# Kernel tuning notes

Measured on AMD Instinct MI355X. Metric: run time of the kernel, lower is better.

The kernel has to match this reference:

```python
import jax, jax.numpy as jnp
import numpy as np

DIM = 128
HEADS = 4
DH = 32
SCALE = DH ** -0.5


def _ln(x, g, b):
    m = x.mean(-1, keepdims=True)
    v = x.var(-1, keepdims=True)
    return (x - m) / jnp.sqrt(v + 1e-5) * g + b


def setup_inputs() -> dict:
    key = jax.random.key(0)
    ks = jax.random.split(key, 16)
    B, N, H, W, HK, WK = 2, 6, 48, 48, 24, 24
    d, hd = DIM, HEADS * DH
    p = lambda k, s: (jax.random.normal(k, s, jnp.float32) * 0.02)
    return {
        "q": jax.random.normal(ks[0], (B, N, d, H, W), jnp.float32),
        "k": jax.random.normal(ks[1], (B, N, d, HK, WK), jnp.float32),
        "v": jax.random.normal(ks[2], (B, N, d, HK, WK), jnp.float32),
        "skip": jax.random.normal(ks[3], (B, d, H, W), jnp.float32),
        "lnq_g": jnp.ones(d), "lnq_b": jnp.zeros(d),
        "Wq": p(ks[4], (d, hd)), "bq": jnp.zeros(hd),
        "lnk_g": jnp.ones(d), "lnk_b": jnp.zeros(d),
        "Wk": p(ks[5], (d, hd)), "bk": jnp.zeros(hd),
        "lnv_g": jnp.ones(d), "lnv_b": jnp.zeros(d),
        "Wv": p(ks[6], (d, hd)), "bv": jnp.zeros(hd),
        "Wp": p(ks[7], (hd, d)), "bp": jnp.zeros(d),
        "pre_g": jnp.ones(d), "pre_b": jnp.zeros(d),
        "W1": p(ks[8], (d, 2 * d)), "b1": jnp.zeros(2 * d),
        "W2": p(ks[9], (2 * d, d)), "b2": jnp.zeros(d),
        "post_g": jnp.ones(d), "post_b": jnp.zeros(d),
    }


def reference(q, k, v, skip, lnq_g, lnq_b, Wq, bq, lnk_g, lnk_b, Wk, bk,
              lnv_g, lnv_b, Wv, bv, Wp, bp, pre_g, pre_b, W1, b1, W2, b2,
              post_g, post_b):
    B, N, d, H, W = q.shape
    _, _, _, HK, WK = k.shape
    Q, K = H * W, HK * WK
    # b n d H W -> b n (H W) d
    qx = q.transpose(0, 1, 3, 4, 2).reshape(B, N, Q, d)
    kx = k.transpose(0, 1, 3, 4, 2).reshape(B, N, K, d)
    vx = v.transpose(0, 1, 3, 4, 2).reshape(B, N * K, d)
    # norm + linear projections
    qp = _ln(qx, lnq_g, lnq_b) @ Wq + bq  # (B,N,Q,HEADS*DH)
    kp = _ln(kx, lnk_g, lnk_b) @ Wk + bk
    vp = _ln(vx, lnv_g, lnv_b) @ Wv + bv  # (B,N*K,HEADS*DH)
    # split heads: b ... (m d) -> (b m) ... d
    qp = qp.reshape(B, N, Q, HEADS, DH).transpose(0, 3, 1, 2, 4).reshape(B * HEADS, N, Q, DH)
    kp = kp.reshape(B, N, K, HEADS, DH).transpose(0, 3, 1, 2, 4).reshape(B * HEADS, N, K, DH)
    vp = vp.reshape(B, N * K, HEADS, DH).transpose(0, 2, 1, 3).reshape(B * HEADS, N * K, DH)
    # per-view scores, then softmax jointly over (n K)
    scores = SCALE * jnp.einsum('bnqd,bnkd->bnqk', qp, kp)
    scores = scores.transpose(0, 2, 1, 3).reshape(B * HEADS, Q, N * K)
    a = jax.nn.softmax(scores, axis=-1)
    out = jnp.einsum('bqk,bkd->bqd', a, vp)  # (B*HEADS, Q, DH)
    # merge heads: (b m) Q d -> b Q (m d)
    z = out.reshape(B, HEADS, Q, DH).transpose(0, 2, 1, 3).reshape(B, Q, HEADS * DH)
    z = z @ Wp + bp
    z = z + skip.transpose(0, 2, 3, 1).reshape(B, Q, d)
    z = _ln(z, pre_g, pre_b)
    z = z + (jax.nn.gelu(z @ W1 + b1, approximate=False) @ W2 + b2)
    z = _ln(z, post_g, post_b)
    return z.reshape(B, H, W, d).transpose(0, 3, 1, 2)
```

## Files before the change

kernel.cpp:

```cpp
#include <hip/hip_runtime.h>
#include <cmath>

#define B_    2
#define N_    6
#define D_    128
#define Q_    2304
#define K_    576
#define NK_   3456
#define HEADS_ 4
#define DH_   32
#define SCALE_ 0.17677669529663687f
#define SCLOG2E_ 0.25504672615621814f

typedef __attribute__((ext_vector_type(8))) short bf16x8;
typedef __attribute__((ext_vector_type(4))) float f32x4;

#if defined(__has_builtin)
#if __has_builtin(__builtin_amdgcn_cvt_pk_bf16_f32)
#define HAS_PK_BF16 1
#endif
#endif

static __device__ __forceinline__ unsigned short f2bf(float f) {
  union { float f; unsigned u; } x; x.f = f;
  unsigned u = x.u + 0x7fffu + ((x.u >> 16) & 1u);
  return (unsigned short)(u >> 16);
}
static __device__ __forceinline__ unsigned pkbf(float a, float b) {
#ifdef HAS_PK_BF16
  typedef __attribute__((ext_vector_type(2))) __bf16 vbf2;
  union { vbf2 v; unsigned u; } cv;
  cv.v = __builtin_amdgcn_cvt_pk_bf16_f32(a, b);
  return cv.u;
#else
  return (unsigned)f2bf(a) | ((unsigned)f2bf(b) << 16);
#endif
}

__global__ __launch_bounds__(256) void k_prep_wt(
    const float* __restrict__ Wq, const float* __restrict__ Wk,
    const float* __restrict__ Wv, const float* __restrict__ Wp,
    const float* __restrict__ W1, const float* __restrict__ W2,
    unsigned short* __restrict__ WTq, unsigned short* __restrict__ WTk,
    unsigned short* __restrict__ WTv, unsigned short* __restrict__ WTp,
    unsigned short* __restrict__ WT1, unsigned short* __restrict__ WT2)
{
  __shared__ float tile[32][33];
  const int wb = blockIdx.x, t = threadIdx.x;
  const float* src; unsigned short* dst; int Kd, J, tl;
  if      (wb < 16) { src = Wq; dst = WTq; Kd = 128; J = 128; tl = wb; }
  else if (wb < 32) { src = Wk; dst = WTk; Kd = 128; J = 128; tl = wb - 16; }
  else if (wb < 48) { src = Wv; dst = WTv; Kd = 128; J = 128; tl = wb - 32; }
  else if (wb < 64) { src = Wp; dst = WTp; Kd = 128; J = 128; tl = wb - 48; }
  else if (wb < 96) { src = W1; dst = WT1; Kd = 128; J = 256; tl = wb - 64; }
  else              { src = W2; dst = WT2; Kd = 256; J = 128; tl = wb - 96; }
  const int njt = J >> 5;
  const int tj = tl % njt, tk = tl / njt;
#pragma unroll
  for (int i = 0; i < 4; ++i) {
    int idx = t + 256 * i;
    int r = idx >> 5, c = idx & 31;
    tile[r][c] = src[(size_t)(tk * 32 + r) * J + tj * 32 + c];
  }
  __syncthreads();
#pragma unroll
  for (int i = 0; i < 2; ++i) {
    int idx = t + 256 * i;
    int rr = idx >> 4, c2 = (idx & 15) << 1;
    *(unsigned*)&dst[(size_t)(tj * 32 + rr) * Kd + tk * 32 + c2] =
        pkbf(tile[c2][rr], tile[c2 + 1][rr]);
  }
}

__global__ __launch_bounds__(256) void k_ln_proj_all(
    const float* __restrict__ qin, const float* __restrict__ kin,
    const float* __restrict__ vin,
    const float* __restrict__ lnq_g, const float* __restrict__ lnq_b,
    const float* __restrict__ lnk_g, const float* __restrict__ lnk_b,
    const float* __restrict__ lnv_g, const float* __restrict__ lnv_b,
    const unsigned short* __restrict__ WTq, const unsigned short* __restrict__ WTk,
    const unsigned short* __restrict__ WTv,
    const float* __restrict__ bq, const float* __restrict__ bk,
    const float* __restrict__ bv,
    unsigned short* __restrict__ QPh, unsigned short* __restrict__ KPh,
    unsigned short* __restrict__ VPTh)
{
  __shared__ float xs[32][132];
  __shared__ unsigned short xh[32][136];
  __shared__ float gs[128], bs[128];
  __shared__ float mu[32], rsd[32];
  const int t = threadIdx.x;
  const int bid = blockIdx.x;

  const float* x; const unsigned short* WT; const float* g; const float* bl;
  const float* bias; int S, blk, mode; float osc;
  if (bid < 864)       { mode = 0; blk = bid;        x = qin; WT = WTq; g = lnq_g; bl = lnq_b; bias = bq; S = Q_; osc = SCLOG2E_; }
  else if (bid < 1080) { mode = 0; blk = bid - 864;  x = kin; WT = WTk; g = lnk_g; bl = lnk_b; bias = bk; S = K_; osc = 1.0f; }
  else                 { mode = 1; blk = bid - 1080; x = vin; WT = WTv; g = lnv_g; bl = lnv_b; bias = bv; S = K_; osc = 1.0f; }
  const int ntile = S >> 5;
  const int o  = blk / ntile;
  const int s0 = (blk % ntile) << 5;

  if (t < 128) { gs[t] = g[t]; bs[t] = bl[t]; }
  const float* xb = x + (size_t)o * 128 * (size_t)S + s0;
#pragma unroll
  for (int i = 0; i < 4; ++i) {
    int idx = t + 256 * i;
    int c = idx >> 3, s4 = (idx & 7) << 2;
    float4 xv = *(const float4*)&xb[(size_t)c * S + s4];
    xs[s4 + 0][c] = xv.x; xs[s4 + 1][c] = xv.y;
    xs[s4 + 2][c] = xv.z; xs[s4 + 3][c] = xv.w;
  }
  __syncthreads();
  {
    int s = t >> 3, l8 = t & 7;
    float sum = 0.f, sq = 0.f;
    for (int c = l8; c < 128; c += 8) { float v = xs[s][c]; sum += v; sq += v * v; }
#pragma unroll
    for (int off = 4; off > 0; off >>= 1) {
      sum += __shfl_down(sum, off, 8);
      sq  += __shfl_down(sq,  off, 8);
    }
    if (l8 == 0) {
      float mth = sum * 0.0078125f;
      float var = sq * 0.0078125f - mth * mth;
      mu[s] = mth; rsd[s] = rsqrtf(var + 1e-5f);
    }
  }
  __syncthreads();
#pragma unroll
  for (int i = 0; i < 8; ++i) {
    int idx = t + 256 * i;
    int s = idx >> 6, c2 = (idx & 63) << 1;
    float y0 = (xs[s][c2]     - mu[s]) * rsd[s] * gs[c2]     + bs[c2];
    float y1 = (xs[s][c2 + 1] - mu[s]) * rsd[s] * gs[c2 + 1] + bs[c2 + 1];
    *(unsigned*)&xh[s][c2] = pkbf(y0, y1);
  }
  __syncthreads();
  const int w = t >> 6, lane = t & 63, quad = lane >> 4, l16 = lane & 15;
  const f32x4 zf = {0.f, 0.f, 0.f, 0.f};
  f32x4 acc[2][2] = {{zf, zf}, {zf, zf}};
#pragma unroll
  for (int kc = 0; kc < 4; ++kc) {
    bf16x8 a0 = *(const bf16x8*)&xh[l16][kc * 32 + quad * 8];
    bf16x8 a1 = *(const bf16x8*)&xh[16 + l16][kc * 32 + quad * 8];
    bf16x8 b0 = *(const bf16x8*)&WT[(size_t)(w * 32 + l16) * 128 + kc * 32 + quad * 8];
    bf16x8 b1 = *(const bf16x8*)&WT[(size_t)(w * 32 + 16 + l16) * 128 + kc * 32 + quad * 8];
    acc[0][0] = __builtin_amdgcn_mfma_f32_16x16x32_bf16(a0, b0, acc[0][0], 0, 0, 0);
    acc[0][1] = __builtin_amdgcn_mfma_f32_16x16x32_bf16(a0, b1, acc[0][1], 0, 0, 0);
    acc[1][0] = __builtin_amdgcn_mfma_f32_16x16x32_bf16(a1, b0, acc[1][0], 0, 0, 0);
    acc[1][1] = __builtin_amdgcn_mfma_f32_16x16x32_bf16(a1, b1, acc[1][1], 0, 0, 0);
  }
  if (mode == 0) {
    unsigned short* outh = (bid < 864) ? QPh : KPh;
    __syncthreads();
#pragma unroll
    for (int mt = 0; mt < 2; ++mt)
#pragma unroll
      for (int nt = 0; nt < 2; ++nt) {
        int col = w * 32 + nt * 16 + l16;
        float bc = bias[col];
#pragma unroll
        for (int r = 0; r < 4; ++r)
          xh[mt * 16 + quad * 4 + r][col] = f2bf((acc[mt][nt][r] + bc) * osc);
      }
    __syncthreads();
#pragma unroll
    for (int i = 0; i < 2; ++i) {
      int s = i * 16 + (t >> 4), c8 = (t & 15) << 3;
      *(uint4*)&outh[((size_t)o * S + s0 + s) * 128 + c8] = *(uint4*)&xh[s][c8];
    }
  } else {
    const int b = o / 6, n = o % 6;
#pragma unroll
    for (int mt = 0; mt < 2; ++mt)
#pragma unroll
      for (int nt = 0; nt < 2; ++nt) {
        int col = w * 32 + nt * 16 + l16;
        int hh = col >> 5, dh = col & 31;
        float bc = bias[col];
        ushort4 pk;
        *(unsigned*)&pk.x = pkbf(acc[mt][nt][0] + bc, acc[mt][nt][1] + bc);
        *(unsigned*)&pk.z = pkbf(acc[mt][nt][2] + bc, acc[mt][nt][3] + bc);
        int s = n * 576 + s0 + mt * 16 + quad * 4;
        *(ushort4*)&VPTh[((size_t)(b * 4 + hh) * 32 + dh) * (size_t)NK_ + s] = pk;
      }
  }
}

__global__ __launch_bounds__(256) void k_attn_mfma(
    const unsigned short* __restrict__ QPh, const unsigned short* __restrict__ KPh,
    const unsigned short* __restrict__ VPTh, float* __restrict__ PO,
    float* __restrict__ Pl)
{
  __shared__ __align__(16) char smem_u[20480];
  typedef unsigned short plds_t[2][2][16][40];
  plds_t* plds = (plds_t*)smem_u;
  float (*ol)[16][32] = (float (*)[16][32])smem_u;
  __shared__ float ll[4][2][4][16];
  const int t = threadIdx.x;
  const int w = t >> 6, lane = t & 63;
  const int quad = lane >> 4, l16 = lane & 15;
  const int qt = blockIdx.x % 72;
  const int rest = blockIdx.x / 72;
  const int bhx = rest >> 1, ks = rest & 1;
  const int bb = bhx >> 2, h = bhx & 3;
  const int q0 = qt << 5;

  const unsigned short* vbase = VPTh + (size_t)bhx * 32 * (size_t)NK_;
  const f32x4 zf = {0.f, 0.f, 0.f, 0.f};
  f32x4 o00 = zf, o01 = zf, o10 = zf, o11 = zf;
  float lsum0 = 0.f, lsum1 = 0.f;
  int buf = 0;

  const int m8 = ks * 4 + w;
  int c0 = (108 * m8) >> 3, c1 = (108 * (m8 + 1)) >> 3;

  while (c0 < c1) {
    const int nn = c0 / 18;
    const int cend = min(c1, (nn + 1) * 18);
    const unsigned short* kb = &KPh[((size_t)(bb * 6 + nn) * K_) * 128 + h * 32];
    const unsigned short* qb = &QPh[((size_t)(bb * 6 + nn) * Q_ + q0) * 128 + h * 32];
    bf16x8 qc0 = *(const bf16x8*)&qb[(size_t)l16 * 128 + quad * 8];
    bf16x8 qc1 = *(const bf16x8*)&qb[(size_t)(16 + l16) * 128 + quad * 8];

    int kl = (c0 - nn * 18) << 5;
    bf16x8 kf0 = *(const bf16x8*)&kb[(size_t)(kl + l16) * 128 + quad * 8];
    bf16x8 kf1 = *(const bf16x8*)&kb[(size_t)(kl + 16 + l16) * 128 + quad * 8];
    const unsigned short* vb = vbase + ((size_t)c0 << 5);
    bf16x8 pv0 = *(const bf16x8*)&vb[(size_t)l16 * NK_ + quad * 8];
    bf16x8 pv1 = *(const bf16x8*)&vb[(size_t)(16 + l16) * NK_ + quad * 8];
    f32x4 s00 = __builtin_amdgcn_mfma_f32_16x16x32_bf16(kf0, qc0, zf, 0, 0, 0);
    f32x4 s01 = __builtin_amdgcn_mfma_f32_16x16x32_bf16(kf1, qc0, zf, 0, 0, 0);
    f32x4 s10 = __builtin_amdgcn_mfma_f32_16x16x32_bf16(kf0, qc1, zf, 0, 0, 0);
    f32x4 s11 = __builtin_amdgcn_mfma_f32_16x16x32_bf16(kf1, qc1, zf, 0, 0, 0);

    for (int kc = c0; kc < cend; ++kc) {
      const int kln = (kc + 1 - nn * 18) << 5;
      bf16x8 nk0 = *(const bf16x8*)&kb[(size_t)(kln + l16) * 128 + quad * 8];
      bf16x8 nk1 = *(const bf16x8*)&kb[(size_t)(kln + 16 + l16) * 128 + quad * 8];
      const unsigned short* vbn = vbase + ((size_t)(kc + 1) << 5);
      bf16x8 nv0 = *(const bf16x8*)&vbn[(size_t)l16 * NK_ + quad * 8];
      bf16x8 nv1 = *(const bf16x8*)&vbn[(size_t)(16 + l16) * NK_ + quad * 8];

      float a00 = exp2f(s00.x), a01 = exp2f(s00.y);
      float a02 = exp2f(s00.z), a03 = exp2f(s00.w);
      float a10 = exp2f(s01.x), a11 = exp2f(s01.y);
      float a12 = exp2f(s01.z), a13 = exp2f(s01.w);
      lsum0 += (a00 + a01 + a02 + a03) + (a10 + a11 + a12 + a13);
      float b00 = exp2f(s10.x), b01 = exp2f(s10.y);
      float b02 = exp2f(s10.z), b03 = exp2f(s10.w);
      float b10 = exp2f(s11.x), b11 = exp2f(s11.y);
      float b12 = exp2f(s11.z), b13 = exp2f(s11.w);
      lsum1 += (b00 + b01 + b02 + b03) + (b10 + b11 + b12 + b13);

      uint2 w0a; w0a.x = pkbf(a00, a01); w0a.y = pkbf(a02, a03);
      uint2 w0b; w0b.x = pkbf(a10, a11); w0b.y = pkbf(a12, a13);
      uint2 w1a; w1a.x = pkbf(b00, b01); w1a.y = pkbf(b02, b03);
      uint2 w1b; w1b.x = pkbf(b10, b11); w1b.y = pkbf(b12, b13);
      *(uint2*)&plds[w][buf][0][l16][quad * 4]      = w0a;
      *(uint2*)&plds[w][buf][0][l16][16 + quad * 4] = w0b;
      *(uint2*)&plds[w][buf][1][l16][quad * 4]      = w1a;
      *(uint2*)&plds[w][buf][1][l16][16 + quad * 4] = w1b;
      bf16x8 pf0 = *(const bf16x8*)&plds[w][buf][0][l16][quad * 8];
      bf16x8 pf1 = *(const bf16x8*)&plds[w][buf][1][l16][quad * 8];

      o00 = __builtin_amdgcn_mfma_f32_16x16x32_bf16(pf0, pv0, o00, 0, 0, 0);
      o01 = __builtin_amdgcn_mfma_f32_16x16x32_bf16(pf0, pv1, o01, 0, 0, 0);
      o10 = __builtin_amdgcn_mfma_f32_16x16x32_bf16(pf1, pv0, o10, 0, 0, 0);
      o11 = __builtin_amdgcn_mfma_f32_16x16x32_bf16(pf1, pv1, o11, 0, 0, 0);

      s00 = __builtin_amdgcn_mfma_f32_16x16x32_bf16(nk0, qc0, zf, 0, 0, 0);
      s01 = __builtin_amdgcn_mfma_f32_16x16x32_bf16(nk1, qc0, zf, 0, 0, 0);
      s10 = __builtin_amdgcn_mfma_f32_16x16x32_bf16(nk0, qc1, zf, 0, 0, 0);
      s11 = __builtin_amdgcn_mfma_f32_16x16x32_bf16(nk1, qc1, zf, 0, 0, 0);
      pv0 = nv0; pv1 = nv1;
      buf ^= 1;
    }
    c0 = cend;
  }

  ll[w][0][quad][l16] = lsum0;
  ll[w][1][quad][l16] = lsum1;
#pragma unroll
  for (int tt = 0; tt < 2; ++tt) {
    __syncthreads();
    f32x4 t0 = tt ? o10 : o00;
    f32x4 t1 = tt ? o11 : o01;
#pragma unroll
    for (int r = 0; r < 4; ++r) {
      ol[w][quad * 4 + r][l16]      = t0[r];
      ol[w][quad * 4 + r][16 + l16] = t1[r];
    }
    __syncthreads();
    const int q = t >> 4, i16 = t & 15, dd = i16 << 1;
    float a0 = 0.f, a1 = 0.f;
#pragma unroll
    for (int ww = 0; ww < 4; ++ww) { a0 += ol[ww][q][dd]; a1 += ol[ww][q][dd + 1]; }
    float2 r2; r2.x = a0; r2.y = a1;
    *(float2*)&PO[(((size_t)ks * 8 + bhx) * Q_ + q0 + tt * 16 + q) * 32 + dd] = r2;
    if (i16 == 0) {
      float l = 0.f;
#pragma unroll
      for (int ww = 0; ww < 4; ++ww)
#pragma unroll
        for (int qq = 0; qq < 4; ++qq) l += ll[ww][tt][qq][q];
      Pl[((size_t)ks * 8 + bhx) * Q_ + q0 + tt * 16 + q] = l;
    }
  }
}

__global__ __launch_bounds__(512) void k_tail(
    const float* __restrict__ PO, const float* __restrict__ Pl,
    const unsigned short* __restrict__ WTp, const float* __restrict__ bp,
    const float* __restrict__ skip,
    const float* __restrict__ pre_g, const float* __restrict__ pre_b,
    const unsigned short* __restrict__ WT1, const float* __restrict__ b1,
    const unsigned short* __restrict__ WT2, const float* __restrict__ b2,
    const float* __restrict__ post_g, const float* __restrict__ post_b,
    float* __restrict__ out)
{
  __shared__ float xs[16][132];
  __shared__ unsigned short xh[16][136];
  __shared__ unsigned short hb[16][264];
  __shared__ float g1s[128], b1s[128], g2s[128], b2s[128];
  __shared__ float mu[16], rsd[16];
  const int t = threadIdx.x;
  const int row0 = blockIdx.x << 4;
  const int bb = row0 / Q_, hw0 = row0 % Q_;
  const int w = t >> 6, lane = t & 63, quad = lane >> 4, l16 = lane & 15;
  const f32x4 zf = {0.f, 0.f, 0.f, 0.f};

  if (t < 128) { g1s[t] = pre_g[t]; b1s[t] = pre_b[t]; g2s[t] = post_g[t]; b2s[t] = post_b[t]; }
#pragma unroll
  for (int i = 0; i < 2; ++i) {
    int idx = t + 512 * i;
    int s = idx >> 6, c2 = (idx & 63) << 1;
    int q = hw0 + s;
    int h = c2 >> 5, dh = c2 & 31;
    size_t bq = (size_t)(bb * 4 + h) * Q_ + q;
    size_t i0 = bq * 32 + dh;
    float2 p0 = *(const float2*)&PO[i0];
    float2 p1 = *(const float2*)&PO[589824 + i0];
    float inv = 1.f / (Pl[bq] + Pl[18432 + bq]);
    *(unsigned*)&xh[s][c2] = pkbf((p0.x + p1.x) * inv, (p0.y + p1.y) * inv);
  }
  __syncthreads();
  {
    f32x4 acc = zf;
    const int col = w * 16 + l16;
#pragma unroll
    for (int kc = 0; kc < 4; ++kc) {
      bf16x8 a0 = *(const bf16x8*)&xh[l16][kc * 32 + quad * 8];
      bf16x8 b0 = *(const bf16x8*)&WTp[(size_t)col * 128 + kc * 32 + quad * 8];
      acc = __builtin_amdgcn_mfma_f32_16x16x32_bf16(a0, b0, acc, 0, 0, 0);
    }
    float bc = bp[col];
    float4 sk = *(const float4*)&skip[((size_t)bb * 128 + col) * Q_ + hw0 + quad * 4];
    xs[quad * 4 + 0][col] = acc[0] + bc + sk.x;
    xs[quad * 4 + 1][col] = acc[1] + bc + sk.y;
    xs[quad * 4 + 2][col] = acc[2] + bc + sk.z;
    xs[quad * 4 + 3][col] = acc[3] + bc + sk.w;
  }
  __syncthreads();
  {
    int s = t >> 5, lg = t & 31;
    float sum = 0.f, sq = 0.f;
    for (int c = lg; c < 128; c += 32) { float v = xs[s][c]; sum += v; sq += v * v; }
#pragma unroll
    for (int off = 16; off > 0; off >>= 1) {
      sum += __shfl_down(sum, off, 32);
      sq  += __shfl_down(sq,  off, 32);
    }
    if (lg == 0) {
      float mth = sum * 0.0078125f;
      float var = sq * 0.0078125f - mth * mth;
      mu[s] = mth; rsd[s] = rsqrtf(var + 1e-5f);
    }
  }
  __syncthreads();
#pragma unroll
  for (int i = 0; i < 2; ++i) {
    int idx = t + 512 * i;
    int s = idx >> 6, c2 = (idx & 63) << 1;
    float y0 = (xs[s][c2]     - mu[s]) * rsd[s] * g1s[c2]     + b1s[c2];
    float y1 = (xs[s][c2 + 1] - mu[s]) * rsd[s] * g1s[c2 + 1] + b1s[c2 + 1];
    xs[s][c2] = y0; xs[s][c2 + 1] = y1;
    *(unsigned*)&xh[s][c2] = pkbf(y0, y1);
  }
  __syncthreads();
  {
#pragma unroll
    for (int nt = 0; nt < 2; ++nt) {
      const int col = w * 32 + nt * 16 + l16;
      f32x4 acc = zf;
#pragma unroll
      for (int kc = 0; kc < 4; ++kc) {
        bf16x8 a0 = *(const bf16x8*)&xh[l16][kc * 32 + quad * 8];
        bf16x8 b0 = *(const bf16x8*)&WT1[(size_t)col * 128 + kc * 32 + quad * 8];
        acc = __builtin_amdgcn_mfma_f32_16x16x32_bf16(a0, b0, acc, 0, 0, 0);
      }
      float bc = b1[col];
#pragma unroll
      for (int r = 0; r < 4; ++r) {
        float hx = acc[r] + bc;
        hb[quad * 4 + r][col] =
            f2bf(0.5f * hx * (1.f + erff(hx * 0.7071067811865476f)));
      }
    }
  }
  __syncthreads();
  {
    f32x4 acc = zf;
    const int col = w * 16 + l16;
#pragma unroll
    for (int kc = 0; kc < 8; ++kc) {
      bf16x8 a0 = *(const bf16x8*)&hb[l16][kc * 32 + quad * 8];
      bf16x8 b0 = *(const bf16x8*)&WT2[(size_t)col * 256 + kc * 32 + quad * 8];
      acc = __builtin_amdgcn_mfma_f32_16x16x32_bf16(a0, b0, acc, 0, 0, 0);
    }
    float bc = b2[col];
#pragma unroll
    for (int r = 0; r < 4; ++r) {
      int row = quad * 4 + r;
      xs[row][col] = acc[r] + bc + xs[row][col];
    }
  }
  __syncthreads();
  {
    int s = t >> 5, lg = t & 31;
    float sum = 0.f, sq = 0.f;
    for (int c = lg; c < 128; c += 32) { float v = xs[s][c]; sum += v; sq += v * v; }
#pragma unroll
    for (int off = 16; off > 0; off >>= 1) {
      sum += __shfl_down(sum, off, 32);
      sq  += __shfl_down(sq,  off, 32);
    }
    if (lg == 0) {
      float mth = sum * 0.0078125f;
      float var = sq * 0.0078125f - mth * mth;
      mu[s] = mth; rsd[s] = rsqrtf(var + 1e-5f);
    }
  }
  __syncthreads();
#pragma unroll
  for (int i = 0; i < 4; ++i) {
    int idx = t + 512 * i;
    int s = idx & 15, c = idx >> 4;
    out[(size_t)bb * (128 * (size_t)Q_) + (size_t)c * Q_ + hw0 + s] =
        (xs[s][c] - mu[s]) * rsd[s] * g2s[c] + b2s[c];
  }
}

extern "C" void kernel_launch(void* const* d_in, const int* in_sizes, int n_in,
                              void* d_out, int out_size, void* d_ws, size_t ws_size,
                              hipStream_t stream) {
  const float* q     = (const float*)d_in[0];
  const float* k     = (const float*)d_in[1];
  const float* v     = (const float*)d_in[2];
  const float* skip  = (const float*)d_in[3];
  const float* lnq_g = (const float*)d_in[4];
  const float* lnq_b = (const float*)d_in[5];
  const float* Wq    = (const float*)d_in[6];
  const float* bq    = (const float*)d_in[7];
  const float* lnk_g = (const float*)d_in[8];
  const float* lnk_b = (const float*)d_in[9];
  const float* Wk    = (const float*)d_in[10];
  const float* bk    = (const float*)d_in[11];
  const float* lnv_g = (const float*)d_in[12];
  const float* lnv_b = (const float*)d_in[13];
  const float* Wv    = (const float*)d_in[14];
  const float* bvv   = (const float*)d_in[15];
  const float* Wp    = (const float*)d_in[16];
  const float* bp    = (const float*)d_in[17];
  const float* pre_g = (const float*)d_in[18];
  const float* pre_b = (const float*)d_in[19];
  const float* W1    = (const float*)d_in[20];
  const float* b1    = (const float*)d_in[21];
  const float* W2    = (const float*)d_in[22];
  const float* b2    = (const float*)d_in[23];
  const float* post_g= (const float*)d_in[24];
  const float* post_b= (const float*)d_in[25];
  float* out = (float*)d_out;

  unsigned short* QPh  = (unsigned short*)d_ws;
  unsigned short* KPh  = QPh + 3538944;
  unsigned short* VPTh = KPh + 884736;
  float* PO  = (float*)(VPTh + 884736);
  float* Pl  = PO + 1179648;
  unsigned short* WTq = (unsigned short*)(Pl + 36864);
  unsigned short* WTk = WTq + 16384;
  unsigned short* WTv = WTk + 16384;
  unsigned short* WTp = WTv + 16384;
  unsigned short* WT1 = WTp + 16384;
  unsigned short* WT2 = WT1 + 32768;

  k_prep_wt<<<dim3(128), dim3(256), 0, stream>>>(Wq, Wk, Wv, Wp, W1, W2,
                                                 WTq, WTk, WTv, WTp, WT1, WT2);
  k_ln_proj_all<<<dim3(1296), dim3(256), 0, stream>>>(
      q, k, v, lnq_g, lnq_b, lnk_g, lnk_b, lnv_g, lnv_b,
      WTq, WTk, WTv, bq, bk, bvv, QPh, KPh, VPTh);
  k_attn_mfma<<<dim3(1152), dim3(256), 0, stream>>>(QPh, KPh, VPTh, PO, Pl);
  k_tail<<<dim3(288), dim3(512), 0, stream>>>(PO, Pl, WTp, bp, skip,
                                              pre_g, pre_b, WT1, b1, WT2, b2,
                                              post_g, post_b, out);
}
```

Before: 176.9 us.

## Replace LDS P transpose with permlane swaps and widen key-split attention

The attention kernel used to pass softmax probabilities from accumulator layout to MFMA operand layout through LDS. It now rearranges them in registers with v_permlane32/16 swap instructions, and it uses raw hardware exp2 and s_setprio around the MFMA block. When the workspace is large enough, the key dimension is split four ways instead of two, which doubles the attention grid. The tail kernel sums a variable number of partial outputs. This trades LDS traffic and waits for more partial-sum traffic and a dependence on workspace size.

```diff
diff --git a/kernel.cpp b/kernel.cpp
--- a/kernel.cpp
+++ b/kernel.cpp
@@ -35,6 +35,13 @@
 #else
   return (unsigned)f2bf(a) | ((unsigned)f2bf(b) << 16);
 #endif
+}
+
+static __device__ __forceinline__ void pl32sw(unsigned &a, unsigned &b) {
+  asm("v_permlane32_swap_b32 %0, %1" : "+v"(a), "+v"(b));
+}
+static __device__ __forceinline__ void pl16sw(unsigned &a, unsigned &b) {
+  asm("v_permlane16_swap_b32 %0, %1" : "+v"(a), "+v"(b));
 }
 
 __global__ __launch_bounds__(256) void k_prep_wt(
@@ -191,19 +198,16 @@
 __global__ __launch_bounds__(256) void k_attn_mfma(
     const unsigned short* __restrict__ QPh, const unsigned short* __restrict__ KPh,
     const unsigned short* __restrict__ VPTh, float* __restrict__ PO,
-    float* __restrict__ Pl)
+    float* __restrict__ Pl, int sh)
 {
-  __shared__ __align__(16) char smem_u[20480];
-  typedef unsigned short plds_t[2][2][16][40];
-  plds_t* plds = (plds_t*)smem_u;
-  float (*ol)[16][32] = (float (*)[16][32])smem_u;
+  __shared__ float ol[4][16][32];
   __shared__ float ll[4][2][4][16];
   const int t = threadIdx.x;
   const int w = t >> 6, lane = t & 63;
   const int quad = lane >> 4, l16 = lane & 15;
   const int qt = blockIdx.x % 72;
   const int rest = blockIdx.x / 72;
-  const int bhx = rest >> 1, ks = rest & 1;
+  const int bhx = rest & 7, ks = rest >> 3;
   const int bb = bhx >> 2, h = bhx & 3;
   const int q0 = qt << 5;
 
@@ -211,10 +215,9 @@
   const f32x4 zf = {0.f, 0.f, 0.f, 0.f};
   f32x4 o00 = zf, o01 = zf, o10 = zf, o11 = zf;
   float lsum0 = 0.f, lsum1 = 0.f;
-  int buf = 0;
 
   const int m8 = ks * 4 + w;
-  int c0 = (108 * m8) >> 3, c1 = (108 * (m8 + 1)) >> 3;
+  int c0 = (108 * m8) >> sh, c1 = (108 * (m8 + 1)) >> sh;
 
   while (c0 < c1) {
     const int nn = c0 / 18;
@@ -243,39 +246,40 @@
       bf16x8 nv0 = *(const bf16x8*)&vbn[(size_t)l16 * NK_ + quad * 8];
       bf16x8 nv1 = *(const bf16x8*)&vbn[(size_t)(16 + l16) * NK_ + quad * 8];
 
-      float a00 = exp2f(s00.x), a01 = exp2f(s00.y);
-      float a02 = exp2f(s00.z), a03 = exp2f(s00.w);
-      float a10 = exp2f(s01.x), a11 = exp2f(s01.y);
-      float a12 = exp2f(s01.z), a13 = exp2f(s01.w);
+      float a00 = __builtin_amdgcn_exp2f(s00.x), a01 = __builtin_amdgcn_exp2f(s00.y);
+      float a02 = __builtin_amdgcn_exp2f(s00.z), a03 = __builtin_amdgcn_exp2f(s00.w);
+      float a10 = __builtin_amdgcn_exp2f(s01.x), a11 = __builtin_amdgcn_exp2f(s01.y);
+      float a12 = __builtin_amdgcn_exp2f(s01.z), a13 = __builtin_amdgcn_exp2f(s01.w);
       lsum0 += (a00 + a01 + a02 + a03) + (a10 + a11 + a12 + a13);
-      float b00 = exp2f(s10.x), b01 = exp2f(s10.y);
-      float b02 = exp2f(s10.z), b03 = exp2f(s10.w);
-      float b10 = exp2f(s11.x), b11 = exp2f(s11.y);
-      float b12 = exp2f(s11.z), b13 = exp2f(s11.w);
+      float b00 = __builtin_amdgcn_exp2f(s10.x), b01 = __builtin_amdgcn_exp2f(s10.y);
+      float b02 = __builtin_amdgcn_exp2f(s10.z), b03 = __builtin_amdgcn_exp2f(s10.w);
+      float b10 = __builtin_amdgcn_exp2f(s11.x), b11 = __builtin_amdgcn_exp2f(s11.y);
+      float b12 = __builtin_amdgcn_exp2f(s11.z), b13 = __builtin_amdgcn_exp2f(s11.w);
       lsum1 += (b00 + b01 + b02 + b03) + (b10 + b11 + b12 + b13);
 
-      uint2 w0a; w0a.x = pkbf(a00, a01); w0a.y = pkbf(a02, a03);
-      uint2 w0b; w0b.x = pkbf(a10, a11); w0b.y = pkbf(a12, a13);
-      uint2 w1a; w1a.x = pkbf(b00, b01); w1a.y = pkbf(b02, b03);
-      uint2 w1b; w1b.x = pkbf(b10, b11); w1b.y = pkbf(b12, b13);
-      *(uint2*)&plds[w][buf][0][l16][quad * 4]      = w0a;
-      *(uint2*)&plds[w][buf][0][l16][16 + quad * 4] = w0b;
-      *(uint2*)&plds[w][buf][1][l16][quad * 4]      = w1a;
-      *(uint2*)&plds[w][buf][1][l16][16 + quad * 4] = w1b;
-      bf16x8 pf0 = *(const bf16x8*)&plds[w][buf][0][l16][quad * 8];
-      bf16x8 pf1 = *(const bf16x8*)&plds[w][buf][1][l16][quad * 8];
-
-      o00 = __builtin_amdgcn_mfma_f32_16x16x32_bf16(pf0, pv0, o00, 0, 0, 0);
-      o01 = __builtin_amdgcn_mfma_f32_16x16x32_bf16(pf0, pv1, o01, 0, 0, 0);
-      o10 = __builtin_amdgcn_mfma_f32_16x16x32_bf16(pf1, pv0, o10, 0, 0, 0);
-      o11 = __builtin_amdgcn_mfma_f32_16x16x32_bf16(pf1, pv1, o11, 0, 0, 0);
-
+      unsigned xA0 = pkbf(a00, a01), xA1 = pkbf(a02, a03);
+      unsigned xB0 = pkbf(a10, a11), xB1 = pkbf(a12, a13);
+      unsigned yA0 = pkbf(b00, b01), yA1 = pkbf(b02, b03);
+      unsigned yB0 = pkbf(b10, b11), yB1 = pkbf(b12, b13);
+      pl32sw(xA0, xB0); pl32sw(xA1, xB1);
+      pl16sw(xA0, xB0); pl16sw(xA1, xB1);
+      pl32sw(yA0, yB0); pl32sw(yA1, yB1);
+      pl16sw(yA0, yB0); pl16sw(yA1, yB1);
+      union { unsigned u[4]; bf16x8 v; } f0, f1;
+      f0.u[0] = xA0; f0.u[1] = xA1; f0.u[2] = xB0; f0.u[3] = xB1;
+      f1.u[0] = yA0; f1.u[1] = yA1; f1.u[2] = yB0; f1.u[3] = yB1;
+
+      __builtin_amdgcn_s_setprio(1);
+      o00 = __builtin_amdgcn_mfma_f32_16x16x32_bf16(f0.v, pv0, o00, 0, 0, 0);
+      o01 = __builtin_amdgcn_mfma_f32_16x16x32_bf16(f0.v, pv1, o01, 0, 0, 0);
+      o10 = __builtin_amdgcn_mfma_f32_16x16x32_bf16(f1.v, pv0, o10, 0, 0, 0);
+      o11 = __builtin_amdgcn_mfma_f32_16x16x32_bf16(f1.v, pv1, o11, 0, 0, 0);
       s00 = __builtin_amdgcn_mfma_f32_16x16x32_bf16(nk0, qc0, zf, 0, 0, 0);
       s01 = __builtin_amdgcn_mfma_f32_16x16x32_bf16(nk1, qc0, zf, 0, 0, 0);
       s10 = __builtin_amdgcn_mfma_f32_16x16x32_bf16(nk0, qc1, zf, 0, 0, 0);
       s11 = __builtin_amdgcn_mfma_f32_16x16x32_bf16(nk1, qc1, zf, 0, 0, 0);
+      __builtin_amdgcn_s_setprio(0);
       pv0 = nv0; pv1 = nv1;
-      buf ^= 1;
     }
     c0 = cend;
   }
@@ -318,7 +322,7 @@
     const unsigned short* __restrict__ WT1, const float* __restrict__ b1,
     const unsigned short* __restrict__ WT2, const float* __restrict__ b2,
     const float* __restrict__ post_g, const float* __restrict__ post_b,
-    float* __restrict__ out)
+    float* __restrict__ out, int nks)
 {
   __shared__ float xs[16][132];
   __shared__ unsigned short xh[16][136];
@@ -340,10 +344,14 @@
     int h = c2 >> 5, dh = c2 & 31;
     size_t bq = (size_t)(bb * 4 + h) * Q_ + q;
     size_t i0 = bq * 32 + dh;
-    float2 p0 = *(const float2*)&PO[i0];
-    float2 p1 = *(const float2*)&PO[589824 + i0];
-    float inv = 1.f / (Pl[bq] + Pl[18432 + bq]);
-    *(unsigned*)&xh[s][c2] = pkbf((p0.x + p1.x) * inv, (p0.y + p1.y) * inv);
+    float px = 0.f, py = 0.f, l = 0.f;
+    for (int p = 0; p < nks; ++p) {
+      float2 pp = *(const float2*)&PO[(size_t)p * 589824 + i0];
+      px += pp.x; py += pp.y;
+      l += Pl[(size_t)p * 18432 + bq];
+    }
+    float inv = 1.f / l;
+    *(unsigned*)&xh[s][c2] = pkbf(px * inv, py * inv);
   }
   __syncthreads();
   {
@@ -483,12 +491,14 @@
   const float* post_b= (const float*)d_in[25];
   float* out = (float*)d_out;
 
+  int nks = 2, sh = 3;
+  if (ws_size >= (size_t)20611072) { nks = 4; sh = 4; }
   unsigned short* QPh  = (unsigned short*)d_ws;
   unsigned short* KPh  = QPh + 3538944;
   unsigned short* VPTh = KPh + 884736;
   float* PO  = (float*)(VPTh + 884736);
-  float* Pl  = PO + 1179648;
-  unsigned short* WTq = (unsigned short*)(Pl + 36864);
+  float* Pl  = PO + (size_t)nks * 589824;
+  unsigned short* WTq = (unsigned short*)(Pl + (size_t)nks * 18432);
   unsigned short* WTk = WTq + 16384;
   unsigned short* WTv = WTk + 16384;
   unsigned short* WTp = WTv + 16384;
@@ -500,8 +510,8 @@
   k_ln_proj_all<<<dim3(1296), dim3(256), 0, stream>>>(
       q, k, v, lnq_g, lnq_b, lnk_g, lnk_b, lnv_g, lnv_b,
       WTq, WTk, WTv, bq, bk, bvv, QPh, KPh, VPTh);
-  k_attn_mfma<<<dim3(1152), dim3(256), 0, stream>>>(QPh, KPh, VPTh, PO, Pl);
+  k_attn_mfma<<<dim3(72 * 8 * nks), dim3(256), 0, stream>>>(QPh, KPh, VPTh, PO, Pl, sh);
   k_tail<<<dim3(288), dim3(512), 0, stream>>>(PO, Pl, WTp, bp, skip,
                                               pre_g, pre_b, WT1, b1, WT2, b2,
-                                              post_g, post_b, out);
-}
+                                              post_g, post_b, out, nks);
+}
```

New measurement: 178.8 us. About the same (+1.0%).
